# Optimization experiments

Hardware: AMD Instinct MI355X
Metric: run time of the kernel (lower is better)

Reference implementation:

```python
import jax, jax.numpy as jnp
import numpy as np


def setup_inputs() -> dict:
    key = jax.random.key(0)
    k1, k2, k3, k4 = jax.random.split(key, 4)
    n, b, h, f = 8, 64, 128, 256
    hs = 64
    x = jax.random.normal(k1, (n, b, h, f), dtype=jnp.float32)
    # torch Linear weights are (out, in); store transposed as (in, out) for x @ W
    Wq = jax.random.normal(k2, (f, hs), dtype=jnp.float32) * (6.0 / (f + hs)) ** 0.5
    Wk = jax.random.normal(k3, (f, hs), dtype=jnp.float32) * (6.0 / (f + hs)) ** 0.5
    Wv = jax.random.normal(k4, (f, hs), dtype=jnp.float32) * (6.0 / (f + hs)) ** 0.5
    return {"x": x, "Wq": Wq, "Wk": Wk, "Wv": Wv}


def reference(x, Wq, Wk, Wv):
    # x: (n, b, h, f). NOTE: scale uses f = n_embd (as in the source), not head_size.
    f = x.shape[-1]
    scale = f ** (-0.5)
    Q = jnp.einsum('nbhf,fd->nbhd', x, Wq)  # (n, b, h, hs)
    K = jnp.einsum('nbhf,fd->nbhd', x, Wk)
    V = jnp.einsum('nbhf,fd->nbhd', x, Wv)
    # alphas[i, j, b, p, q] = sum_d Q[j,b,p,d] * K[i,b,q,d] * scale
    scores = jnp.einsum('jbpd,ibqd->ijbpq', Q, K) * scale  # (n, n, b, h, h)
    alphas = jax.nn.softmax(scores, axis=-1)
    # out[i, j, b, p, d] = sum_q alphas[i,j,b,p,q] V[i,b,q,d]; then sum over i
    o = jnp.einsum('ijbpq,ibqd->jbpd', alphas, V)  # (n, b, h, hs)
    return o
```

## Files before the change

### kernel.cpp

```cpp
#include <hip/hip_runtime.h>
#include <cstdint>

#define N_SEQ 8
#define B_DIM 64
#define H_DIM 128
#define F_DIM 256
#define HS 64

typedef __attribute__((ext_vector_type(8))) short short8;
typedef __attribute__((ext_vector_type(4))) float floatx4;

__device__ __forceinline__ ushort f2bf(float f) {
    union { float f; uint32_t u; } v; v.f = f;
    uint32_t r = v.u + 0x7FFF + ((v.u >> 16) & 1);
    return (ushort)(r >> 16);
}

__device__ __forceinline__ void async_ld16(const ushort* g, ushort* lds) {
    __builtin_amdgcn_global_load_lds(
        (const __attribute__((address_space(1))) unsigned int*)g,
        (__attribute__((address_space(3))) unsigned int*)lds,
        16, 0, 0);
}

__global__ __launch_bounds__(256) void prep_w(
    const float* __restrict__ Wq, const float* __restrict__ Wk,
    const float* __restrict__ Wv, ushort* __restrict__ Wtb)
{
    const int n = blockIdx.x;
    const float* W = (n < 64) ? Wq : (n < 128) ? Wk : Wv;
    const int c = n & 63;
    const int k = threadIdx.x;
    Wtb[n * 256 + k] = f2bf(W[k * 64 + c]);
}

#define XS_STRIDE 264
__global__ __launch_bounds__(256, 4) void proj_mfma(
    const float* __restrict__ x, const ushort* __restrict__ Wtb,
    ushort* __restrict__ Qb, ushort* __restrict__ Kb, ushort* __restrict__ Vtb)
{
    __shared__ ushort xs[64 * XS_STRIDE];
    const int t = threadIdx.x;
    const int blk = blockIdx.x;
    const int64_t row0 = (int64_t)blk * 64;

    const float4* xg = (const float4*)(x + row0 * F_DIM);
    #pragma unroll
    for (int u = 0; u < 8; ++u) {
        const int idx = t + 256 * u;
        const int row = idx >> 5;
        const int c8 = (idx & 31) * 8;
        const float4 a = xg[idx * 2];
        const float4 b = xg[idx * 2 + 1];
        *(ushort4*)&xs[row * XS_STRIDE + c8] =
            make_ushort4(f2bf(a.x), f2bf(a.y), f2bf(a.z), f2bf(a.w));
        *(ushort4*)&xs[row * XS_STRIDE + c8 + 4] =
            make_ushort4(f2bf(b.x), f2bf(b.y), f2bf(b.z), f2bf(b.w));
    }
    __syncthreads();

    const int w = t >> 6, lane = t & 63;
    const int q16 = lane >> 4, l16 = lane & 15;
    const int n0 = w * 48;

    floatx4 acc[4][3];
    #pragma unroll
    for (int mt = 0; mt < 4; ++mt)
        #pragma unroll
        for (int nt = 0; nt < 3; ++nt) acc[mt][nt] = (floatx4){0.f, 0.f, 0.f, 0.f};

    short8 nb[3];
    #pragma unroll
    for (int nt = 0; nt < 3; ++nt)
        nb[nt] = *(const short8*)&Wtb[(n0 + nt * 16 + l16) * 256 + q16 * 8];

    for (int ks = 0; ks < 8; ++ks) {
        short8 cur[3];
        #pragma unroll
        for (int nt = 0; nt < 3; ++nt) cur[nt] = nb[nt];
        if (ks < 7) {
            #pragma unroll
            for (int nt = 0; nt < 3; ++nt)
                nb[nt] = *(const short8*)&Wtb[(n0 + nt * 16 + l16) * 256 + (ks + 1) * 32 + q16 * 8];
        }
        #pragma unroll
        for (int mt = 0; mt < 4; ++mt) {
            const short8 afr = *(const short8*)&xs[(mt * 16 + l16) * XS_STRIDE + ks * 32 + q16 * 8];
            #pragma unroll
            for (int nt = 0; nt < 3; ++nt)
                acc[mt][nt] = __builtin_amdgcn_mfma_f32_16x16x32_bf16(afr, cur[nt], acc[mt][nt], 0, 0, 0);
        }
    }

    const float qscale = 0.0625f * 1.44269504f;
    #pragma unroll
    for (int mt = 0; mt < 4; ++mt) {
        const int64_t g = row0 + mt * 16 + q16 * 4;
        #pragma unroll
        for (int nt = 0; nt < 3; ++nt) {
            const int ntb = n0 + nt * 16;
            const int n = ntb + l16;
            if (ntb < 64) {
                #pragma unroll
                for (int r = 0; r < 4; ++r)
                    Qb[(g + r) * 64 + n] = f2bf(acc[mt][nt][r] * qscale);
            } else if (ntb < 128) {
                #pragma unroll
                for (int r = 0; r < 4; ++r)
                    Kb[(g + r) * 64 + (n - 64)] = f2bf(acc[mt][nt][r]);
            } else {
                const int d = n - 128;
                const int ib = (int)(g >> 7);
                const int h = (int)(g & 127);
                *(ushort4*)&Vtb[((int64_t)(ib * 64 + d)) * 128 + h] =
                    make_ushort4(f2bf(acc[mt][nt][0]), f2bf(acc[mt][nt][1]),
                                 f2bf(acc[mt][nt][2]), f2bf(acc[mt][nt][3]));
            }
        }
    }
}

#define PT_STRIDE 40
__global__ __launch_bounds__(256, 2) void attn_mfma(
    const ushort* __restrict__ Qb, const ushort* __restrict__ Kb,
    const ushort* __restrict__ Vtb, float* __restrict__ out)
{
    __shared__ ushort Ks[2][8192];
    __shared__ ushort Ps[4][2][16 * PT_STRIDE];

    const int t = threadIdx.x;
    const int blk = blockIdx.x;
    const int b  = ((blk & 7) << 3) | ((blk >> 3) & 7);
    const int j  = blk >> 6;
    const int jb = j * 64 + b;

    const int w = t >> 6, lane = t & 63;
    const int q16 = lane >> 4, l16 = lane & 15;

    int koff[4], ldsoff[4];
    #pragma unroll
    for (int u = 0; u < 4; ++u) {
        const int fi = w * 4 + u;
        koff[u] = ((fi & 7) * 16 + l16) * 64 + (fi >> 3) * 32 + q16 * 8;
        ldsoff[u] = fi * 512;
    }
    const int voff0 = l16 * 128 + q16 * 8;

    const int prow = jb * H_DIM + w * 16 + l16;
    short8 qa[2][2];
    #pragma unroll
    for (int hh = 0; hh < 2; ++hh)
        #pragma unroll
        for (int ks = 0; ks < 2; ++ks)
            qa[hh][ks] = *(const short8*)&Qb[(prow + hh * 64) * 64 + ks * 32 + q16 * 8];

    floatx4 of[2][4];
    #pragma unroll
    for (int hh = 0; hh < 2; ++hh)
        #pragma unroll
        for (int mt = 0; mt < 4; ++mt) of[hh][mt] = (floatx4){0.f, 0.f, 0.f, 0.f};

    {
        const ushort* kg = Kb + ((0 * B_DIM + b) << 13);
        #pragma unroll
        for (int u = 0; u < 4; ++u) {
            const int lo = __builtin_amdgcn_readfirstlane(ldsoff[u]);
            async_ld16(kg + koff[u], &Ks[0][lo]);
        }
    }

    for (int i = 0; i < N_SEQ; ++i) {
        const int buf = i & 1;
        __syncthreads();

        if (i < N_SEQ - 1) {
            const ushort* kg = Kb + (((i + 1) * B_DIM + b) << 13);
            #pragma unroll
            for (int u = 0; u < 4; ++u) {
                const int lo = __builtin_amdgcn_readfirstlane(ldsoff[u]);
                async_ld16(kg + koff[u], &Ks[buf ^ 1][lo]);
            }
        }

        const ushort* vg = Vtb + ((i * B_DIM + b) << 13);
        short8 av[4][4];
        #pragma unroll
        for (int kq = 0; kq < 4; ++kq)
            #pragma unroll
            for (int mt = 0; mt < 4; ++mt)
                av[kq][mt] = *(const short8*)&vg[voff0 + mt * 2048 + kq * 32];

        floatx4 sf[2][8];
        #pragma unroll
        for (int hh = 0; hh < 2; ++hh)
            #pragma unroll
            for (int nt = 0; nt < 8; ++nt) sf[hh][nt] = (floatx4){0.f, 0.f, 0.f, 0.f};
        #pragma unroll
        for (int ks = 0; ks < 2; ++ks)
            #pragma unroll
            for (int nt = 0; nt < 8; ++nt) {
                const short8 ak = *(const short8*)&Ks[buf][(ks * 8 + nt) * 512 + lane * 8];
                sf[0][nt] = __builtin_amdgcn_mfma_f32_16x16x32_bf16(ak, qa[0][ks], sf[0][nt], 0, 0, 0);
                sf[1][nt] = __builtin_amdgcn_mfma_f32_16x16x32_bf16(ak, qa[1][ks], sf[1][nt], 0, 0, 0);
            }

        float inv[2];
        #pragma unroll
        for (int hh = 0; hh < 2; ++hh) {
            float l = 0.f;
            #pragma unroll
            for (int nt = 0; nt < 8; ++nt)
                #pragma unroll
                for (int r = 0; r < 4; ++r) {
                    sf[hh][nt][r] = __builtin_amdgcn_exp2f(sf[hh][nt][r]);
                    l += sf[hh][nt][r];
                }
            l += __shfl_xor(l, 16);
            l += __shfl_xor(l, 32);
            inv[hh] = __builtin_amdgcn_rcpf(l);
        }

        floatx4 tmp[2][4];
        #pragma unroll
        for (int hh = 0; hh < 2; ++hh)
            #pragma unroll
            for (int mt = 0; mt < 4; ++mt) tmp[hh][mt] = (floatx4){0.f, 0.f, 0.f, 0.f};

        #pragma unroll
        for (int kq = 0; kq < 4; ++kq) {
            #pragma unroll
            for (int hh = 0; hh < 2; ++hh)
                #pragma unroll
                for (int tt = 0; tt < 2; ++tt) {
                    const int nt = kq * 2 + tt;
                    *(ushort4*)&Ps[w][hh][l16 * PT_STRIDE + tt * 16 + q16 * 4] =
                        make_ushort4(f2bf(sf[hh][nt][0]), f2bf(sf[hh][nt][1]),
                                     f2bf(sf[hh][nt][2]), f2bf(sf[hh][nt][3]));
                }
            const short8 bp0 = *(const short8*)&Ps[w][0][l16 * PT_STRIDE + q16 * 8];
            const short8 bp1 = *(const short8*)&Ps[w][1][l16 * PT_STRIDE + q16 * 8];
            #pragma unroll
            for (int mt = 0; mt < 4; ++mt) {
                tmp[0][mt] = __builtin_amdgcn_mfma_f32_16x16x32_bf16(av[kq][mt], bp0, tmp[0][mt], 0, 0, 0);
                tmp[1][mt] = __builtin_amdgcn_mfma_f32_16x16x32_bf16(av[kq][mt], bp1, tmp[1][mt], 0, 0, 0);
            }
        }

        #pragma unroll
        for (int hh = 0; hh < 2; ++hh)
            #pragma unroll
            for (int mt = 0; mt < 4; ++mt)
                #pragma unroll
                for (int r = 0; r < 4; ++r)
                    of[hh][mt][r] += tmp[hh][mt][r] * inv[hh];
    }

    #pragma unroll
    for (int hh = 0; hh < 2; ++hh)
        #pragma unroll
        for (int mt = 0; mt < 4; ++mt)
            *(float4*)&out[(int64_t)(prow + hh * 64) * HS + mt * 16 + q16 * 4] =
                make_float4(of[hh][mt][0], of[hh][mt][1], of[hh][mt][2], of[hh][mt][3]);
}

extern "C" void kernel_launch(void* const* d_in, const int* in_sizes, int n_in,
                              void* d_out, int out_size, void* d_ws, size_t ws_size,
                              hipStream_t stream)
{
    const float* x  = (const float*)d_in[0];
    const float* Wq = (const float*)d_in[1];
    const float* Wk = (const float*)d_in[2];
    const float* Wv = (const float*)d_in[3];
    float* out = (float*)d_out;

    const size_t qkv = (size_t)N_SEQ * B_DIM * H_DIM * HS;
    ushort* Qb  = (ushort*)d_ws;
    ushort* Kb  = Qb + qkv;
    ushort* Vtb = Kb + qkv;
    ushort* Wtb = Vtb + qkv;

    prep_w<<<192, 256, 0, stream>>>(Wq, Wk, Wv, Wtb);
    proj_mfma<<<(N_SEQ * B_DIM * H_DIM) / 64, 256, 0, stream>>>(x, Wtb, Qb, Kb, Vtb);
    attn_mfma<<<N_SEQ * B_DIM, 256, 0, stream>>>(Qb, Kb, Vtb, out);
}
```

Baseline: 156.6 us.

## Split attention keys across wave pairs with 512-thread blocks and LDS-staged V

The attention kernel now launches 512 threads per block. Waves are paired so that each pair covers 32 query rows, and the two waves in a pair each take half of the 128 keys. V is no longer read straight from global memory into registers; it is prefetched asynchronously into double-buffered LDS alongside K. Partial softmax denominators and output accumulators are combined across the wave pair through LDS, which adds an extra barrier per iteration and a final reduction step. The aim is more waves in flight to hide latency and lower register pressure, at the cost of more synchronisation and LDS traffic.

```diff
diff --git a/kernel.cpp b/kernel.cpp
--- a/kernel.cpp
+++ b/kernel.cpp
@@ -121,12 +121,14 @@
 }
 
 #define PT_STRIDE 40
-__global__ __launch_bounds__(256, 2) void attn_mfma(
+__global__ __launch_bounds__(512, 4) void attn_mfma(
     const ushort* __restrict__ Qb, const ushort* __restrict__ Kb,
     const ushort* __restrict__ Vtb, float* __restrict__ out)
 {
-    __shared__ ushort Ks[2][8192];
-    __shared__ ushort Ps[4][2][16 * PT_STRIDE];
+    __shared__ __align__(16) ushort Ks[2][2][4096];
+    __shared__ __align__(16) ushort Vt[2][2][4096];
+    __shared__ __align__(16) ushort Ps[8][16 * PT_STRIDE];
+    __shared__ float Ls[2][4][2][64];
 
     const int t = threadIdx.x;
     const int blk = blockIdx.x;
@@ -135,37 +137,39 @@
     const int jb = j * 64 + b;
 
     const int w = t >> 6, lane = t & 63;
+    const int pg = w >> 1, kg = w & 1;
     const int q16 = lane >> 4, l16 = lane & 15;
 
-    int koff[4], ldsoff[4];
-    #pragma unroll
-    for (int u = 0; u < 4; ++u) {
-        const int fi = w * 4 + u;
-        koff[u] = ((fi & 7) * 16 + l16) * 64 + (fi >> 3) * 32 + q16 * 8;
-        ldsoff[u] = fi * 512;
-    }
-    const int voff0 = l16 * 128 + q16 * 8;
-
-    const int prow = jb * H_DIM + w * 16 + l16;
+    int koff[2], voff[2], lk[2];
+    #pragma unroll
+    for (int u = 0; u < 2; ++u) {
+        const int fi = pg * 2 + u;
+        koff[u] = (kg * 64 + (fi & 3) * 16 + l16) * 64 + (fi >> 2) * 32 + q16 * 8;
+        voff[u] = ((fi & 3) * 16 + l16) * 128 + kg * 64 + (fi >> 2) * 32 + q16 * 8;
+        lk[u] = __builtin_amdgcn_readfirstlane(fi * 512);
+    }
+
+    const int prow = jb * H_DIM + pg * 32 + l16;
     short8 qa[2][2];
     #pragma unroll
-    for (int hh = 0; hh < 2; ++hh)
+    for (int pt = 0; pt < 2; ++pt)
         #pragma unroll
         for (int ks = 0; ks < 2; ++ks)
-            qa[hh][ks] = *(const short8*)&Qb[(prow + hh * 64) * 64 + ks * 32 + q16 * 8];
-
-    floatx4 of[2][4];
-    #pragma unroll
-    for (int hh = 0; hh < 2; ++hh)
-        #pragma unroll
-        for (int mt = 0; mt < 4; ++mt) of[hh][mt] = (floatx4){0.f, 0.f, 0.f, 0.f};
+            qa[pt][ks] = *(const short8*)&Qb[(prow + pt * 16) * 64 + ks * 32 + q16 * 8];
+
+    floatx4 of[4][2];
+    #pragma unroll
+    for (int mt = 0; mt < 4; ++mt)
+        #pragma unroll
+        for (int pt = 0; pt < 2; ++pt) of[mt][pt] = (floatx4){0.f, 0.f, 0.f, 0.f};
 
     {
-        const ushort* kg = Kb + ((0 * B_DIM + b) << 13);
-        #pragma unroll
-        for (int u = 0; u < 4; ++u) {
-            const int lo = __builtin_amdgcn_readfirstlane(ldsoff[u]);
-            async_ld16(kg + koff[u], &Ks[0][lo]);
+        const ushort* kgp = Kb + ((0 * B_DIM + b) << 13);
+        const ushort* vgp = Vtb + ((0 * B_DIM + b) << 13);
+        #pragma unroll
+        for (int u = 0; u < 2; ++u) {
+            async_ld16(kgp + koff[u], &Ks[kg][0][lk[u]]);
+            async_ld16(vgp + voff[u], &Vt[kg][0][lk[u]]);
         }
     }
 
@@ -174,93 +178,107 @@
         __syncthreads();
 
         if (i < N_SEQ - 1) {
-            const ushort* kg = Kb + (((i + 1) * B_DIM + b) << 13);
-            #pragma unroll
-            for (int u = 0; u < 4; ++u) {
-                const int lo = __builtin_amdgcn_readfirstlane(ldsoff[u]);
-                async_ld16(kg + koff[u], &Ks[buf ^ 1][lo]);
+            const ushort* kgp = Kb + (((i + 1) * B_DIM + b) << 13);
+            const ushort* vgp = Vtb + (((i + 1) * B_DIM + b) << 13);
+            #pragma unroll
+            for (int u = 0; u < 2; ++u) {
+                async_ld16(kgp + koff[u], &Ks[kg][buf ^ 1][lk[u]]);
+                async_ld16(vgp + voff[u], &Vt[kg][buf ^ 1][lk[u]]);
             }
         }
 
-        const ushort* vg = Vtb + ((i * B_DIM + b) << 13);
-        short8 av[4][4];
-        #pragma unroll
-        for (int kq = 0; kq < 4; ++kq)
-            #pragma unroll
-            for (int mt = 0; mt < 4; ++mt)
-                av[kq][mt] = *(const short8*)&vg[voff0 + mt * 2048 + kq * 32];
-
-        floatx4 sf[2][8];
-        #pragma unroll
-        for (int hh = 0; hh < 2; ++hh)
-            #pragma unroll
-            for (int nt = 0; nt < 8; ++nt) sf[hh][nt] = (floatx4){0.f, 0.f, 0.f, 0.f};
-        #pragma unroll
-        for (int ks = 0; ks < 2; ++ks)
-            #pragma unroll
-            for (int nt = 0; nt < 8; ++nt) {
-                const short8 ak = *(const short8*)&Ks[buf][(ks * 8 + nt) * 512 + lane * 8];
-                sf[0][nt] = __builtin_amdgcn_mfma_f32_16x16x32_bf16(ak, qa[0][ks], sf[0][nt], 0, 0, 0);
-                sf[1][nt] = __builtin_amdgcn_mfma_f32_16x16x32_bf16(ak, qa[1][ks], sf[1][nt], 0, 0, 0);
-            }
-
-        float inv[2];
-        #pragma unroll
-        for (int hh = 0; hh < 2; ++hh) {
+        float lsum[2];
+        floatx4 tmp[4][2];
+        #pragma unroll
+        for (int mt = 0; mt < 4; ++mt)
+            #pragma unroll
+            for (int pt = 0; pt < 2; ++pt) tmp[mt][pt] = (floatx4){0.f, 0.f, 0.f, 0.f};
+
+        #pragma unroll
+        for (int pt = 0; pt < 2; ++pt) {
+            floatx4 sf[4];
+            #pragma unroll
+            for (int kt = 0; kt < 4; ++kt) sf[kt] = (floatx4){0.f, 0.f, 0.f, 0.f};
+            #pragma unroll
+            for (int ks = 0; ks < 2; ++ks)
+                #pragma unroll
+                for (int kt = 0; kt < 4; ++kt) {
+                    const short8 ak = *(const short8*)&Ks[kg][buf][(ks * 4 + kt) * 512 + lane * 8];
+                    sf[kt] = __builtin_amdgcn_mfma_f32_16x16x32_bf16(ak, qa[pt][ks], sf[kt], 0, 0, 0);
+                }
+
             float l = 0.f;
             #pragma unroll
-            for (int nt = 0; nt < 8; ++nt)
+            for (int kt = 0; kt < 4; ++kt)
                 #pragma unroll
                 for (int r = 0; r < 4; ++r) {
-                    sf[hh][nt][r] = __builtin_amdgcn_exp2f(sf[hh][nt][r]);
-                    l += sf[hh][nt][r];
+                    sf[kt][r] = __builtin_amdgcn_exp2f(sf[kt][r]);
+                    l += sf[kt][r];
                 }
             l += __shfl_xor(l, 16);
             l += __shfl_xor(l, 32);
-            inv[hh] = __builtin_amdgcn_rcpf(l);
-        }
-
-        floatx4 tmp[2][4];
-        #pragma unroll
-        for (int hh = 0; hh < 2; ++hh)
-            #pragma unroll
-            for (int mt = 0; mt < 4; ++mt) tmp[hh][mt] = (floatx4){0.f, 0.f, 0.f, 0.f};
-
-        #pragma unroll
-        for (int kq = 0; kq < 4; ++kq) {
-            #pragma unroll
-            for (int hh = 0; hh < 2; ++hh)
+            lsum[pt] = l;
+
+            #pragma unroll
+            for (int kq = 0; kq < 2; ++kq) {
                 #pragma unroll
                 for (int tt = 0; tt < 2; ++tt) {
-                    const int nt = kq * 2 + tt;
-                    *(ushort4*)&Ps[w][hh][l16 * PT_STRIDE + tt * 16 + q16 * 4] =
-                        make_ushort4(f2bf(sf[hh][nt][0]), f2bf(sf[hh][nt][1]),
-                                     f2bf(sf[hh][nt][2]), f2bf(sf[hh][nt][3]));
+                    const int kt = kq * 2 + tt;
+                    *(ushort4*)&Ps[w][l16 * PT_STRIDE + tt * 16 + q16 * 4] =
+                        make_ushort4(f2bf(sf[kt][0]), f2bf(sf[kt][1]),
+                                     f2bf(sf[kt][2]), f2bf(sf[kt][3]));
                 }
-            const short8 bp0 = *(const short8*)&Ps[w][0][l16 * PT_STRIDE + q16 * 8];
-            const short8 bp1 = *(const short8*)&Ps[w][1][l16 * PT_STRIDE + q16 * 8];
-            #pragma unroll
-            for (int mt = 0; mt < 4; ++mt) {
-                tmp[0][mt] = __builtin_amdgcn_mfma_f32_16x16x32_bf16(av[kq][mt], bp0, tmp[0][mt], 0, 0, 0);
-                tmp[1][mt] = __builtin_amdgcn_mfma_f32_16x16x32_bf16(av[kq][mt], bp1, tmp[1][mt], 0, 0, 0);
+                const short8 bp = *(const short8*)&Ps[w][l16 * PT_STRIDE + q16 * 8];
+                #pragma unroll
+                for (int mt = 0; mt < 4; ++mt) {
+                    const short8 av = *(const short8*)&Vt[kg][buf][(kq * 4 + mt) * 512 + lane * 8];
+                    tmp[mt][pt] = __builtin_amdgcn_mfma_f32_16x16x32_bf16(av, bp, tmp[mt][pt], 0, 0, 0);
+                }
             }
-        }
-
-        #pragma unroll
-        for (int hh = 0; hh < 2; ++hh)
+
+            Ls[kg][pg][pt][q16 * 16 + l16] = lsum[pt];
+        }
+
+        __syncthreads();
+
+        #pragma unroll
+        for (int pt = 0; pt < 2; ++pt) {
+            const float inv = __builtin_amdgcn_rcpf(
+                lsum[pt] + Ls[kg ^ 1][pg][pt][q16 * 16 + l16]);
             #pragma unroll
             for (int mt = 0; mt < 4; ++mt)
                 #pragma unroll
                 for (int r = 0; r < 4; ++r)
-                    of[hh][mt][r] += tmp[hh][mt][r] * inv[hh];
-    }
-
-    #pragma unroll
-    for (int hh = 0; hh < 2; ++hh)
+                    of[mt][pt][r] += tmp[mt][pt][r] * inv;
+        }
+    }
+
+    __syncthreads();
+    float* Ob = (float*)&Ks[0][0][0];
+    if (kg == 1) {
         #pragma unroll
         for (int mt = 0; mt < 4; ++mt)
-            *(float4*)&out[(int64_t)(prow + hh * 64) * HS + mt * 16 + q16 * 4] =
-                make_float4(of[hh][mt][0], of[hh][mt][1], of[hh][mt][2], of[hh][mt][3]);
+            #pragma unroll
+            for (int pt = 0; pt < 2; ++pt)
+                *(floatx4*)&Ob[(pg * 8 + mt * 2 + pt) * 256 + lane * 4] = of[mt][pt];
+    }
+    __syncthreads();
+    if (kg == 0) {
+        #pragma unroll
+        for (int mt = 0; mt < 4; ++mt)
+            #pragma unroll
+            for (int pt = 0; pt < 2; ++pt) {
+                const floatx4 o2 = *(const floatx4*)&Ob[(pg * 8 + mt * 2 + pt) * 256 + lane * 4];
+                #pragma unroll
+                for (int r = 0; r < 4; ++r) of[mt][pt][r] += o2[r];
+            }
+        #pragma unroll
+        for (int pt = 0; pt < 2; ++pt)
+            #pragma unroll
+            for (int mt = 0; mt < 4; ++mt)
+                *(float4*)&out[(int64_t)(prow + pt * 16) * HS + mt * 16 + q16 * 4] =
+                    make_float4(of[mt][pt][0], of[mt][pt][1], of[mt][pt][2], of[mt][pt][3]);
+    }
 }
 
 extern "C" void kernel_launch(void* const* d_in, const int* in_sizes, int n_in,
@@ -281,5 +299,5 @@
 
     prep_w<<<192, 256, 0, stream>>>(Wq, Wk, Wv, Wtb);
     proj_mfma<<<(N_SEQ * B_DIM * H_DIM) / 64, 256, 0, stream>>>(x, Wtb, Qb, Kb, Vtb);
-    attn_mfma<<<N_SEQ * B_DIM, 256, 0, stream>>>(Qb, Kb, Vtb, out);
-}
+    attn_mfma<<<N_SEQ * B_DIM, 512, 0, stream>>>(Qb, Kb, Vtb, out);
+}
```

After: 148.5 us. 5.2% less time.
